# Kernel tuning notes

Hardware: AMD Instinct MI355X
Metric: run time of the kernel (lower is better)

## Reference

```python
import jax, jax.numpy as jnp
import numpy as np

B, S, D, P, NQ = 8, 2048, 1024, 256, 8192


def setup_inputs() -> dict:
    key = jax.random.key(0)
    ks = jax.random.split(key, 8)
    return {
        "flag": 0,
        "encoded_input": jax.random.normal(ks[0], (B, S, D), dtype=jnp.float32),
        "start_ids_1": jax.random.randint(ks[1], (NQ,), 0, S, dtype=jnp.int32),
        "end_ids_1": jax.random.randint(ks[2], (NQ,), 0, S, dtype=jnp.int32),
        "query_batch_idx": jax.random.randint(ks[3], (NQ,), 0, B, dtype=jnp.int32),
        "start_ids_2": jax.random.randint(ks[4], (NQ,), 0, S, dtype=jnp.int32),
        "end_ids_2": jax.random.randint(ks[5], (NQ,), 0, S, dtype=jnp.int32),
        "W": jax.random.normal(ks[6], (D, P), dtype=jnp.float32) * 0.02,
        "b": jnp.zeros((P,), dtype=jnp.float32),
    }


def _gather_spans(h, qb, s, e):
    # span_repr[b, i, j] = concat(h[b, i], h[b, j]) for j >= i, else 0.
    # Direct gather instead of building the O(seq^2) table.
    rep = jnp.concatenate([h[qb, s], h[qb, e]], axis=-1)  # [NQ, 2*P]
    valid = (e >= s).astype(rep.dtype)[:, None]
    return rep * valid


def reference(flag, encoded_input, start_ids_1, end_ids_1, query_batch_idx,
              start_ids_2, end_ids_2, W, b):
    h = encoded_input @ W + b  # [B, S, P] (use_proj=True)
    res1 = _gather_spans(h, query_batch_idx, start_ids_1, end_ids_1)
    res2 = _gather_spans(h, query_batch_idx, start_ids_2, end_ids_2)
    return (res1, res2)
```

## Files before the change

### kernel.cpp

```cpp
#include <hip/hip_runtime.h>
#include <hip/hip_bf16.h>
#include <stdint.h>

#define S_LEN 2048
#define D_DIM 1024
#define P_DIM 256
#define NQ_   8192
#define M_TOT 16384

#define BM 32
#define BN 256
#define BK 64
#define CAP 32
#define HS  260

typedef __attribute__((ext_vector_type(4))) float  f32x4;
typedef __attribute__((ext_vector_type(8))) __bf16 bf16x8;

__device__ __forceinline__ void async16(const void* g, void* l) {
    __builtin_amdgcn_global_load_lds(
        (const __attribute__((address_space(1))) uint32_t*)g,
        (__attribute__((address_space(3))) uint32_t*)l, 16, 0, 0);
}

__global__ __launch_bounds__(1024) void wt_kernel(const float* __restrict__ W,
                                                  __bf16* __restrict__ WT,
                                                  int* __restrict__ cnt) {
    __shared__ __bf16 tile[32][33];
    const int k0 = blockIdx.x * 32;
    const int n0 = blockIdx.y * 32;
    const int tx = threadIdx.x, ty = threadIdx.y;
    const int g = (blockIdx.y * gridDim.x + blockIdx.x) * 1024 + ty * 32 + tx;
    if (g < M_TOT) cnt[g] = 0;
    tile[ty][tx] = (__bf16)W[(k0 + ty) * P_DIM + (n0 + tx)];
    __syncthreads();
    WT[(n0 + ty) * D_DIM + (k0 + tx)] = tile[tx][ty];
}

__global__ __launch_bounds__(256) void index_build(const int* __restrict__ s1,
                                                   const int* __restrict__ e1,
                                                   const int* __restrict__ s2,
                                                   const int* __restrict__ e2,
                                                   const int* __restrict__ qb,
                                                   int* __restrict__ cnt,
                                                   int* __restrict__ bucket) {
    const int q = blockIdx.x * 256 + threadIdx.x;
    const int b = qb[q];
    int s = s1[q], e = e1[q];
    if (e >= s) {
        int r = b * S_LEN + s;
        int k = atomicAdd(&cnt[r], 1); if (k < CAP) bucket[r * CAP + k] = (q << 2);
        r = b * S_LEN + e;
        k = atomicAdd(&cnt[r], 1);     if (k < CAP) bucket[r * CAP + k] = (q << 2) | 1;
    }
    s = s2[q]; e = e2[q];
    if (e >= s) {
        int r = b * S_LEN + s;
        int k = atomicAdd(&cnt[r], 1); if (k < CAP) bucket[r * CAP + k] = (q << 2) | 2;
        r = b * S_LEN + e;
        k = atomicAdd(&cnt[r], 1);     if (k < CAP) bucket[r * CAP + k] = (q << 2) | 3;
    }
}

__global__ __launch_bounds__(256) void invalid_zero(const int* __restrict__ s1,
                                                    const int* __restrict__ e1,
                                                    const int* __restrict__ s2,
                                                    const int* __restrict__ e2,
                                                    float* __restrict__ out) {
    const int grp  = threadIdx.x >> 6;
    const int gl   = threadIdx.x & 63;
    const int pair = blockIdx.x * 4 + grp;
    const int q    = pair & (NQ_ - 1);
    const int set  = pair >> 13;
    const int s = set ? s2[q] : s1[q];
    const int e = set ? e2[q] : e1[q];
    if (e >= s) return;
    const float4 z = make_float4(0.f, 0.f, 0.f, 0.f);
    float* dst = out + (size_t)set * (NQ_ * 512) + (size_t)q * 512;
    ((float4*)dst)[gl]      = z;
    ((float4*)dst)[gl + 64] = z;
}

__global__ __launch_bounds__(256, 2) void gemm_kernel(const float*  __restrict__ A,
                                                      const __bf16* __restrict__ WT,
                                                      const float*  __restrict__ bias,
                                                      const int*    __restrict__ cnt,
                                                      const int*    __restrict__ bucket,
                                                      float*        __restrict__ out) {
    __shared__ __align__(16) char smem[2 * BM * BK * 2 + 2 * BN * BK * 2];
    __shared__ int s_cnt[32];
    __shared__ int s_off[33];
    __shared__ int elist[32 * CAP];

    const int tid = threadIdx.x;
    const int w   = tid >> 6;
    const int l   = tid & 63;
    const int lm  = l & 15;
    const int q   = l >> 4;

    const int m0 = blockIdx.x * BM;

    auto bufA = [&](int buf) -> __bf16* { return (__bf16*)smem + buf * (BM * BK); };
    auto bufB = [&](int buf) -> __bf16* { return (__bf16*)(smem + 2 * BM * BK * 2) + buf * (BN * BK); };

    const int brow_l = l >> 3;
    const int bc     = (l & 7) ^ (brow_l & 7);

    auto stageB = [&](int buf, int k0) {
        __bf16* B = bufB(buf);
        #pragma unroll
        for (int j = 0; j < 8; ++j) {
            const int r   = w * 8 + j;
            const int row = r * 8 + brow_l;
            const __bf16* g = WT + (size_t)row * D_DIM + k0 + bc * 8;
            async16(g, B + r * 512);
        }
    };

    const int arow = tid >> 3;
    const int acp  = tid & 7;
    const int ac   = acp ^ (arow & 7);
    const float* agp = A + (size_t)(m0 + arow) * D_DIM + ac * 8;

    float4 fa0, fa1;
    auto loadA = [&](int k0) {
        fa0 = *(const float4*)(agp + k0);
        fa1 = *(const float4*)(agp + k0 + 4);
    };
    auto writeA = [&](int buf) {
        bf16x8 v;
        v[0] = (__bf16)fa0.x; v[1] = (__bf16)fa0.y; v[2] = (__bf16)fa0.z; v[3] = (__bf16)fa0.w;
        v[4] = (__bf16)fa1.x; v[5] = (__bf16)fa1.y; v[6] = (__bf16)fa1.z; v[7] = (__bf16)fa1.w;
        *(bf16x8*)(bufA(buf) + arow * BK + acp * 8) = v;
    };

    f32x4 acc[2][4] = {};

    auto compute = [&](int buf) {
        const __bf16* Ab = bufA(buf);
        const __bf16* Bb = bufB(buf);
        #pragma unroll
        for (int kh = 0; kh < 2; ++kh) {
            const int pos = ((kh * 4 + q) ^ (lm & 7)) * 8;
            bf16x8 af[2], bfr[4];
            #pragma unroll
            for (int mi = 0; mi < 2; ++mi)
                af[mi] = *(const bf16x8*)(Ab + (mi * 16 + lm) * BK + pos);
            #pragma unroll
            for (int ni = 0; ni < 4; ++ni)
                bfr[ni] = *(const bf16x8*)(Bb + (w * 64 + ni * 16 + lm) * BK + pos);
            #pragma unroll
            for (int mi = 0; mi < 2; ++mi)
                #pragma unroll
                for (int ni = 0; ni < 4; ++ni)
                    acc[mi][ni] = __builtin_amdgcn_mfma_f32_16x16x32_bf16(
                        af[mi], bfr[ni], acc[mi][ni], 0, 0, 0);
        }
    };

    loadA(0);
    stageB(0, 0);
    writeA(0);
    __syncthreads();

    #pragma unroll 1
    for (int p = 0; p < 7; ++p) {
        const int k1 = (2 * p + 1) * BK, k2 = (2 * p + 2) * BK;
        loadA(k1); stageB(1, k1);
        __builtin_amdgcn_sched_barrier(0);
        compute(0);
        __builtin_amdgcn_sched_barrier(0);
        writeA(1);
        __syncthreads();
        loadA(k2); stageB(0, k2);
        __builtin_amdgcn_sched_barrier(0);
        compute(1);
        __builtin_amdgcn_sched_barrier(0);
        writeA(0);
        __syncthreads();
    }
    {
        const int k1 = 15 * BK;
        loadA(k1); stageB(1, k1);
        __builtin_amdgcn_sched_barrier(0);
        compute(0);
        __builtin_amdgcn_sched_barrier(0);
        writeA(1);
        __syncthreads();
    }
    compute(1);

    __syncthreads();
    float* hs = (float*)smem;

    if (tid < 32) { int c = cnt[m0 + tid]; s_cnt[tid] = c < CAP ? c : CAP; }

    #pragma unroll
    for (int ni = 0; ni < 4; ++ni) {
        const int col = w * 64 + ni * 16 + lm;
        const float bv = bias[col];
        #pragma unroll
        for (int mi = 0; mi < 2; ++mi) {
            const int rbase = mi * 16 + q * 4;
            #pragma unroll
            for (int r = 0; r < 4; ++r)
                hs[(rbase + r) * HS + col] = acc[mi][ni][r] + bv;
        }
    }
    __syncthreads();
    if (tid == 0) {
        int a = 0;
        #pragma unroll 1
        for (int i = 0; i < 32; ++i) { s_off[i] = a; a += s_cnt[i]; }
        s_off[32] = a;
    }
    __syncthreads();
    if (tid < 32) {
        const int o = s_off[tid], c = s_cnt[tid];
        const int* bk = bucket + (size_t)(m0 + tid) * CAP;
        for (int k = 0; k < c; ++k)
            elist[o + k] = (tid << 15) | (bk[k] & 0x7fff);
    }
    __syncthreads();

    const int E   = s_off[32];
    const int grp = tid >> 6;
    const int gl  = tid & 63;
    #pragma unroll 1
    for (int j = grp; j < E; j += 4) {
        const int ent  = elist[j];
        const int rl   = ent >> 15;
        const int code = ent & 0x7fff;
        const int qq   = code >> 2;
        const int st   = (code >> 1) & 1;
        const int hf   = code & 1;
        const float4 v = *(const float4*)&hs[rl * HS + gl * 4];
        *(float4*)(out + (size_t)st * (NQ_ * 512) + (size_t)qq * 512 + hf * 256 + gl * 4) = v;
    }
}

extern "C" void kernel_launch(void* const* d_in, const int* in_sizes, int n_in,
                              void* d_out, int out_size, void* d_ws, size_t ws_size,
                              hipStream_t stream) {
    const float* A    = (const float*)d_in[1];
    const int*   s1   = (const int*)  d_in[2];
    const int*   e1   = (const int*)  d_in[3];
    const int*   qb   = (const int*)  d_in[4];
    const int*   s2   = (const int*)  d_in[5];
    const int*   e2   = (const int*)  d_in[6];
    const float* W    = (const float*)d_in[7];
    const float* bias = (const float*)d_in[8];
    float*       out  = (float*)d_out;

    __bf16* WT     = (__bf16*)d_ws;
    int*    cnt    = (int*)((char*)d_ws + (1 << 20));
    int*    bucket = (int*)((char*)d_ws + (1 << 20) + (1 << 16));

    wt_kernel    <<<dim3(32, 8), dim3(32, 32), 0, stream>>>(W, WT, cnt);
    index_build  <<<dim3(NQ_ / 256), dim3(256), 0, stream>>>(s1, e1, s2, e2, qb, cnt, bucket);
    invalid_zero <<<dim3(2 * NQ_ / 4), dim3(256), 0, stream>>>(s1, e1, s2, e2, out);
    gemm_kernel  <<<dim3(M_TOT / BM), dim3(256), 0, stream>>>(A, WT, bias, cnt, bucket, out);
}
```

Measured before the change: 145.7 us.

## Double GEMM row tile to 64 and fuse index build with invalid-span zeroing

The GEMM row tile grows from 32 to 64 rows, so each workgroup computes a 64x256 output tile with 16 MFMA accumulators per wave. This reuses each staged WT tile across twice as many rows and halves the number of workgroups, at the cost of more registers and LDS and a launch bound of 1. Separately, the index-building and invalid-span zeroing kernels are merged into one launch, which uses a wave ballot to cooperatively zero the invalid output rows. Together this removes one kernel launch and the redundant index reads.

```diff
diff --git a/kernel.cpp b/kernel.cpp
--- a/kernel.cpp
+++ b/kernel.cpp
@@ -8,7 +8,7 @@
 #define NQ_   8192
 #define M_TOT 16384
 
-#define BM 32
+#define BM 64
 #define BN 256
 #define BK 64
 #define CAP 32
@@ -37,60 +37,51 @@
     WT[(n0 + ty) * D_DIM + (k0 + tx)] = tile[tx][ty];
 }
 
-__global__ __launch_bounds__(256) void index_build(const int* __restrict__ s1,
-                                                   const int* __restrict__ e1,
-                                                   const int* __restrict__ s2,
-                                                   const int* __restrict__ e2,
-                                                   const int* __restrict__ qb,
-                                                   int* __restrict__ cnt,
-                                                   int* __restrict__ bucket) {
-    const int q = blockIdx.x * 256 + threadIdx.x;
-    const int b = qb[q];
-    int s = s1[q], e = e1[q];
-    if (e >= s) {
-        int r = b * S_LEN + s;
-        int k = atomicAdd(&cnt[r], 1); if (k < CAP) bucket[r * CAP + k] = (q << 2);
-        r = b * S_LEN + e;
-        k = atomicAdd(&cnt[r], 1);     if (k < CAP) bucket[r * CAP + k] = (q << 2) | 1;
-    }
-    s = s2[q]; e = e2[q];
-    if (e >= s) {
-        int r = b * S_LEN + s;
-        int k = atomicAdd(&cnt[r], 1); if (k < CAP) bucket[r * CAP + k] = (q << 2) | 2;
-        r = b * S_LEN + e;
-        k = atomicAdd(&cnt[r], 1);     if (k < CAP) bucket[r * CAP + k] = (q << 2) | 3;
-    }
-}
-
-__global__ __launch_bounds__(256) void invalid_zero(const int* __restrict__ s1,
-                                                    const int* __restrict__ e1,
-                                                    const int* __restrict__ s2,
-                                                    const int* __restrict__ e2,
-                                                    float* __restrict__ out) {
-    const int grp  = threadIdx.x >> 6;
-    const int gl   = threadIdx.x & 63;
-    const int pair = blockIdx.x * 4 + grp;
-    const int q    = pair & (NQ_ - 1);
-    const int set  = pair >> 13;
-    const int s = set ? s2[q] : s1[q];
-    const int e = set ? e2[q] : e1[q];
-    if (e >= s) return;
+__global__ __launch_bounds__(256) void index_zero(const int* __restrict__ s1,
+                                                  const int* __restrict__ e1,
+                                                  const int* __restrict__ s2,
+                                                  const int* __restrict__ e2,
+                                                  const int* __restrict__ qb,
+                                                  int* __restrict__ cnt,
+                                                  int* __restrict__ bucket,
+                                                  float* __restrict__ out) {
+    const int q    = blockIdx.x * 256 + threadIdx.x;
+    const int lane = threadIdx.x & 63;
+    const int bqw  = blockIdx.x * 256 + (threadIdx.x & ~63);
+    const int b    = qb[q];
     const float4 z = make_float4(0.f, 0.f, 0.f, 0.f);
-    float* dst = out + (size_t)set * (NQ_ * 512) + (size_t)q * 512;
-    ((float4*)dst)[gl]      = z;
-    ((float4*)dst)[gl + 64] = z;
-}
-
-__global__ __launch_bounds__(256, 2) void gemm_kernel(const float*  __restrict__ A,
+    #pragma unroll
+    for (int set = 0; set < 2; ++set) {
+        const int s = set ? s2[q] : s1[q];
+        const int e = set ? e2[q] : e1[q];
+        if (e >= s) {
+            int r = b * S_LEN + s;
+            int k = atomicAdd(&cnt[r], 1); if (k < CAP) bucket[r * CAP + k] = (q << 2) | (set << 1);
+            r = b * S_LEN + e;
+            k = atomicAdd(&cnt[r], 1);     if (k < CAP) bucket[r * CAP + k] = (q << 2) | (set << 1) | 1;
+        }
+        unsigned long long mask = __ballot(e < s);
+        while (mask) {
+            const int j = __ffsll(mask) - 1;
+            mask &= mask - 1;
+            const int qz = bqw + j;
+            float4* dst = (float4*)(out + (size_t)set * (NQ_ * 512) + (size_t)qz * 512);
+            dst[lane]      = z;
+            dst[lane + 64] = z;
+        }
+    }
+}
+
+__global__ __launch_bounds__(256, 1) void gemm_kernel(const float*  __restrict__ A,
                                                       const __bf16* __restrict__ WT,
                                                       const float*  __restrict__ bias,
                                                       const int*    __restrict__ cnt,
                                                       const int*    __restrict__ bucket,
                                                       float*        __restrict__ out) {
     __shared__ __align__(16) char smem[2 * BM * BK * 2 + 2 * BN * BK * 2];
-    __shared__ int s_cnt[32];
-    __shared__ int s_off[33];
-    __shared__ int elist[32 * CAP];
+    __shared__ int s_cnt[64];
+    __shared__ int s_off[65];
+    __shared__ int elist[64 * CAP];
 
     const int tid = threadIdx.x;
     const int w   = tid >> 6;
@@ -117,24 +108,29 @@
         }
     };
 
-    const int arow = tid >> 3;
-    const int acp  = tid & 7;
-    const int ac   = acp ^ (arow & 7);
-    const float* agp = A + (size_t)(m0 + arow) * D_DIM + ac * 8;
-
-    float4 fa0, fa1;
+    const int arow = tid >> 2;
+    const int ac   = tid & 3;
+    const float* agp = A + (size_t)(m0 + arow) * D_DIM + ac * 16;
+    const int p0 = ((2 * ac)     ^ (arow & 7)) * 8;
+    const int p1 = ((2 * ac + 1) ^ (arow & 7)) * 8;
+
+    float4 fa[4];
     auto loadA = [&](int k0) {
-        fa0 = *(const float4*)(agp + k0);
-        fa1 = *(const float4*)(agp + k0 + 4);
+        #pragma unroll
+        for (int i = 0; i < 4; ++i) fa[i] = *(const float4*)(agp + k0 + 4 * i);
     };
     auto writeA = [&](int buf) {
-        bf16x8 v;
-        v[0] = (__bf16)fa0.x; v[1] = (__bf16)fa0.y; v[2] = (__bf16)fa0.z; v[3] = (__bf16)fa0.w;
-        v[4] = (__bf16)fa1.x; v[5] = (__bf16)fa1.y; v[6] = (__bf16)fa1.z; v[7] = (__bf16)fa1.w;
-        *(bf16x8*)(bufA(buf) + arow * BK + acp * 8) = v;
-    };
-
-    f32x4 acc[2][4] = {};
+        bf16x8 v0, v1;
+        v0[0] = (__bf16)fa[0].x; v0[1] = (__bf16)fa[0].y; v0[2] = (__bf16)fa[0].z; v0[3] = (__bf16)fa[0].w;
+        v0[4] = (__bf16)fa[1].x; v0[5] = (__bf16)fa[1].y; v0[6] = (__bf16)fa[1].z; v0[7] = (__bf16)fa[1].w;
+        v1[0] = (__bf16)fa[2].x; v1[1] = (__bf16)fa[2].y; v1[2] = (__bf16)fa[2].z; v1[3] = (__bf16)fa[2].w;
+        v1[4] = (__bf16)fa[3].x; v1[5] = (__bf16)fa[3].y; v1[6] = (__bf16)fa[3].z; v1[7] = (__bf16)fa[3].w;
+        __bf16* Ab = bufA(buf) + arow * BK;
+        *(bf16x8*)(Ab + p0) = v0;
+        *(bf16x8*)(Ab + p1) = v1;
+    };
+
+    f32x4 acc[4][4] = {};
 
     auto compute = [&](int buf) {
         const __bf16* Ab = bufA(buf);
@@ -142,15 +138,15 @@
         #pragma unroll
         for (int kh = 0; kh < 2; ++kh) {
             const int pos = ((kh * 4 + q) ^ (lm & 7)) * 8;
-            bf16x8 af[2], bfr[4];
-            #pragma unroll
-            for (int mi = 0; mi < 2; ++mi)
+            bf16x8 af[4], bfr[4];
+            #pragma unroll
+            for (int mi = 0; mi < 4; ++mi)
                 af[mi] = *(const bf16x8*)(Ab + (mi * 16 + lm) * BK + pos);
             #pragma unroll
             for (int ni = 0; ni < 4; ++ni)
                 bfr[ni] = *(const bf16x8*)(Bb + (w * 64 + ni * 16 + lm) * BK + pos);
             #pragma unroll
-            for (int mi = 0; mi < 2; ++mi)
+            for (int mi = 0; mi < 4; ++mi)
                 #pragma unroll
                 for (int ni = 0; ni < 4; ++ni)
                     acc[mi][ni] = __builtin_amdgcn_mfma_f32_16x16x32_bf16(
@@ -193,14 +189,14 @@
     __syncthreads();
     float* hs = (float*)smem;
 
-    if (tid < 32) { int c = cnt[m0 + tid]; s_cnt[tid] = c < CAP ? c : CAP; }
+    if (tid < 64) { int c = cnt[m0 + tid]; s_cnt[tid] = c < CAP ? c : CAP; }
 
     #pragma unroll
     for (int ni = 0; ni < 4; ++ni) {
         const int col = w * 64 + ni * 16 + lm;
         const float bv = bias[col];
         #pragma unroll
-        for (int mi = 0; mi < 2; ++mi) {
+        for (int mi = 0; mi < 4; ++mi) {
             const int rbase = mi * 16 + q * 4;
             #pragma unroll
             for (int r = 0; r < 4; ++r)
@@ -211,11 +207,11 @@
     if (tid == 0) {
         int a = 0;
         #pragma unroll 1
-        for (int i = 0; i < 32; ++i) { s_off[i] = a; a += s_cnt[i]; }
-        s_off[32] = a;
-    }
-    __syncthreads();
-    if (tid < 32) {
+        for (int i = 0; i < 64; ++i) { s_off[i] = a; a += s_cnt[i]; }
+        s_off[64] = a;
+    }
+    __syncthreads();
+    if (tid < 64) {
         const int o = s_off[tid], c = s_cnt[tid];
         const int* bk = bucket + (size_t)(m0 + tid) * CAP;
         for (int k = 0; k < c; ++k)
@@ -223,7 +219,7 @@
     }
     __syncthreads();
 
-    const int E   = s_off[32];
+    const int E   = s_off[64];
     const int grp = tid >> 6;
     const int gl  = tid & 63;
     #pragma unroll 1
@@ -256,8 +252,7 @@
     int*    cnt    = (int*)((char*)d_ws + (1 << 20));
     int*    bucket = (int*)((char*)d_ws + (1 << 20) + (1 << 16));
 
-    wt_kernel    <<<dim3(32, 8), dim3(32, 32), 0, stream>>>(W, WT, cnt);
-    index_build  <<<dim3(NQ_ / 256), dim3(256), 0, stream>>>(s1, e1, s2, e2, qb, cnt, bucket);
-    invalid_zero <<<dim3(2 * NQ_ / 4), dim3(256), 0, stream>>>(s1, e1, s2, e2, out);
-    gemm_kernel  <<<dim3(M_TOT / BM), dim3(256), 0, stream>>>(A, WT, bias, cnt, bucket, out);
-}
+    wt_kernel  <<<dim3(32, 8), dim3(32, 32), 0, stream>>>(W, WT, cnt);
+    index_zero <<<dim3(NQ_ / 256), dim3(256), 0, stream>>>(s1, e1, s2, e2, qb, cnt, bucket, out);
+    gemm_kernel<<<dim3(M_TOT / BM), dim3(256), 0, stream>>>(A, WT, bias, cnt, bucket, out);
+}
```

Measured after the change: 147.9 us. Within noise of the previous version (+1.5%).
